# Performance work log

Measured on AMD Instinct MI355X. Metric: run time of the kernel, lower is better.

Reference implementation:

```python
import jax, jax.numpy as jnp
import numpy as np

N_NODES = 100000
N_EDGES = 600000
D = 128
N_GRAPHS = 128
EPS_GIN = 0.0      # GINConv eps (train_eps=False -> constant)
EPS_LN = 1e-5      # LayerNorm eps


def setup_inputs() -> dict:
    key = jax.random.key(0)
    ks = jax.random.split(key, 8)
    x = jax.random.normal(ks[0], (N_NODES, D), dtype=jnp.float32)
    edge_index = jax.random.randint(ks[1], (2, N_EDGES), 0, N_NODES, dtype=jnp.int64)
    batch = jnp.sort(jax.random.randint(ks[2], (N_NODES,), 0, N_GRAPHS, dtype=jnp.int64))
    # GIN update MLP: Linear(D,D) -> ReLU -> Linear(D,D)
    s = 1.0 / np.sqrt(D)
    W1 = jax.random.uniform(ks[3], (D, D), jnp.float32, -s, s)
    b1 = jax.random.uniform(ks[4], (D,), jnp.float32, -s, s)
    W2 = jax.random.uniform(ks[5], (D, D), jnp.float32, -s, s)
    b2 = jax.random.uniform(ks[6], (D,), jnp.float32, -s, s)
    # node LayerNorm affine params
    gamma = jnp.ones((D,), jnp.float32)
    beta = jnp.zeros((D,), jnp.float32)
    return {"x": x, "W1": W1, "b1": b1, "W2": W2, "b2": b2,
            "gamma": gamma, "beta": beta, "edge_index": edge_index, "batch": batch}


def reference(x, W1, b1, W2, b2, gamma, beta, edge_index, batch):
    src, dst = edge_index[0], edge_index[1]
    # AGGREGATION: m_i = sum_{j in N(i)} x_j  (scatter-sum of gathered source feats)
    m = jax.ops.segment_sum(x[src], dst, num_segments=N_NODES)  # [N, D]
    # UPDATE: MLP((1+eps)*x + m)
    h = (1.0 + EPS_GIN) * x + m
    h = jax.nn.relu(h @ W1 + b1) @ W2 + b2
    # node-mode LayerNorm: normalize each node over its feature dimension
    mu = jnp.mean(h, axis=-1, keepdims=True)
    var = jnp.mean((h - mu) ** 2, axis=-1, keepdims=True)
    return (h - mu) * jax.lax.rsqrt(var + EPS_LN) * gamma + beta
```

## Files before the change

kernel.cpp:

```cpp
#include <hip/hip_runtime.h>

#define NN 100000
#define NE 600000
#define DD 128
#define SCAN_BLOCKS 100
#define SCAN_CHUNK  1000

typedef __bf16 bf16x8 __attribute__((ext_vector_type(8)));
typedef float f32x4 __attribute__((ext_vector_type(4)));
typedef unsigned short ushort8 __attribute__((ext_vector_type(8)));

static __device__ __forceinline__ unsigned short f2bf(float f) {
    return __builtin_bit_cast(unsigned short, (__bf16)f);
}

__global__ void prep_w_kernel(const float* __restrict__ W1, const float* __restrict__ W2,
                              unsigned short* __restrict__ w1t, unsigned short* __restrict__ w2t) {
    int t = blockIdx.x * blockDim.x + threadIdx.x;
    int k = t >> 7, n = t & 127;
    w1t[n * DD + k] = f2bf(W1[k * DD + n]);
    w2t[n * DD + k] = f2bf(W2[k * DD + n]);
}

__global__ void hist_kernel(const int* __restrict__ ei, int* __restrict__ deg) {
    int e = blockIdx.x * blockDim.x + threadIdx.x;
    if (e < NE) atomicAdd(&deg[ei[NE + e]], 1);
}

__global__ void scanA_kernel(const int* __restrict__ deg, int* __restrict__ bsum) {
    __shared__ int red[256];
    int b = blockIdx.x, t = threadIdx.x;
    int base = b * SCAN_CHUNK;
    int s = 0;
    for (int i = t; i < SCAN_CHUNK; i += 256) s += deg[base + i];
    red[t] = s;
    __syncthreads();
    for (int off = 128; off > 0; off >>= 1) {
        if (t < off) red[t] += red[t + off];
        __syncthreads();
    }
    if (t == 0) bsum[b] = red[0];
}

__global__ void scanB_kernel(const int* __restrict__ bsum, int* __restrict__ boff) {
    __shared__ int s[128];
    int t = threadIdx.x;
    int v0 = (t < SCAN_BLOCKS) ? bsum[t] : 0;
    s[t] = v0;
    __syncthreads();
    for (int off = 1; off < 128; off <<= 1) {
        int u = (t >= off) ? s[t - off] : 0;
        __syncthreads();
        s[t] += u;
        __syncthreads();
    }
    if (t < SCAN_BLOCKS) boff[t] = s[t] - v0;
}

__global__ void scanC_kernel(const int* __restrict__ deg, const int* __restrict__ boff,
                             int* __restrict__ row_ptr, int* __restrict__ cursor) {
    __shared__ int s[1024];
    int b = blockIdx.x, t = threadIdx.x;
    int i = b * SCAN_CHUNK + t;
    int v = (t < SCAN_CHUNK) ? deg[i] : 0;
    s[t] = v;
    __syncthreads();
    for (int off = 1; off < 1024; off <<= 1) {
        int u = (t >= off) ? s[t - off] : 0;
        __syncthreads();
        s[t] += u;
        __syncthreads();
    }
    if (t < SCAN_CHUNK) {
        int excl = boff[b] + s[t] - v;
        row_ptr[i] = excl;
        cursor[i]  = excl;
        if (i == NN - 1) row_ptr[NN] = excl + v;
    }
}

__global__ void fill_kernel(const int* __restrict__ ei, int* __restrict__ cursor,
                            int* __restrict__ eidx) {
    int e = blockIdx.x * blockDim.x + threadIdx.x;
    if (e >= NE) return;
    int src = ei[e];
    int dst = ei[NE + e];
    int pos = atomicAdd(&cursor[dst], 1);
    eidx[pos] = src;
}

__global__ void gather_kernel(const float* __restrict__ x, const int* __restrict__ row_ptr,
                              const int* __restrict__ eidx, float* __restrict__ m) {
    int t = blockIdx.x * blockDim.x + threadIdx.x;
    int node = t >> 5;
    int j = (t & 31) * 4;
    if (node >= NN) return;
    int beg = row_ptr[node], end = row_ptr[node + 1];
    float4 acc = {0.f, 0.f, 0.f, 0.f};
    for (int e = beg; e < end; ++e) {
        int src = eidx[e];
        float4 v = *(const float4*)(x + (size_t)src * DD + j);
        acc.x += v.x; acc.y += v.y; acc.z += v.z; acc.w += v.w;
    }
    *(float4*)(m + (size_t)node * DD + j) = acc;
}

__launch_bounds__(256)
__global__ void fused_mlp_ln_kernel(const float* __restrict__ x, const float* __restrict__ m,
                                    const unsigned short* __restrict__ w1t,
                                    const unsigned short* __restrict__ w2t,
                                    const float* __restrict__ b1, const float* __restrict__ b2,
                                    const float* __restrict__ gamma, const float* __restrict__ beta,
                                    float* __restrict__ out) {
    __shared__ __align__(16) unsigned short h1[4][16][136];

    const int tid  = threadIdx.x;
    const int w    = tid >> 6;
    const int l    = tid & 63;
    const int lcol = l & 15;
    const int g    = l >> 4;
    const int m0   = blockIdx.x * 64 + w * 16;

    int arow = m0 + lcol;
    if (arow >= NN) arow = NN - 1;
    const float* xr = x + (size_t)arow * DD;
    const float* mr = m + (size_t)arow * DD;
    bf16x8 afrag[4];
    #pragma unroll
    for (int t = 0; t < 4; ++t) {
        int k0 = t * 32 + g * 8;
        float4 xa = *(const float4*)(xr + k0);
        float4 xb = *(const float4*)(xr + k0 + 4);
        float4 ma = *(const float4*)(mr + k0);
        float4 mb = *(const float4*)(mr + k0 + 4);
        bf16x8 a;
        a[0] = (__bf16)(xa.x + ma.x); a[1] = (__bf16)(xa.y + ma.y);
        a[2] = (__bf16)(xa.z + ma.z); a[3] = (__bf16)(xa.w + ma.w);
        a[4] = (__bf16)(xb.x + mb.x); a[5] = (__bf16)(xb.y + mb.y);
        a[6] = (__bf16)(xb.z + mb.z); a[7] = (__bf16)(xb.w + mb.w);
        afrag[t] = a;
    }

    f32x4 acc[8];
    #pragma unroll
    for (int nt = 0; nt < 8; ++nt) {
        float bv = b1[nt * 16 + lcol];
        acc[nt] = (f32x4){bv, bv, bv, bv};
    }
    #pragma unroll
    for (int t = 0; t < 4; ++t) {
        int k0 = t * 32 + g * 8;
        #pragma unroll
        for (int nt = 0; nt < 8; ++nt) {
            ushort8 bu = *(const ushort8*)(w1t + (size_t)(nt * 16 + lcol) * DD + k0);
            acc[nt] = __builtin_amdgcn_mfma_f32_16x16x32_bf16(
                afrag[t], __builtin_bit_cast(bf16x8, bu), acc[nt], 0, 0, 0);
        }
    }

    #pragma unroll
    for (int nt = 0; nt < 8; ++nt)
        #pragma unroll
        for (int r = 0; r < 4; ++r) {
            float v = fmaxf(acc[nt][r], 0.f);
            h1[w][g * 4 + r][nt * 16 + lcol] = f2bf(v);
        }
    __syncthreads();

    bf16x8 a2[4];
    #pragma unroll
    for (int t = 0; t < 4; ++t) {
        int k0 = t * 32 + g * 8;
        a2[t] = __builtin_bit_cast(bf16x8, *(const ushort8*)(&h1[w][lcol][k0]));
    }

    #pragma unroll
    for (int nt = 0; nt < 8; ++nt) {
        float bv = b2[nt * 16 + lcol];
        acc[nt] = (f32x4){bv, bv, bv, bv};
    }
    #pragma unroll
    for (int t = 0; t < 4; ++t) {
        #pragma unroll
        for (int nt = 0; nt < 8; ++nt) {
            ushort8 bu = *(const ushort8*)(w2t + (size_t)(nt * 16 + lcol) * DD + (t * 32 + g * 8));
            acc[nt] = __builtin_amdgcn_mfma_f32_16x16x32_bf16(
                a2[t], __builtin_bit_cast(bf16x8, bu), acc[nt], 0, 0, 0);
        }
    }

    float gmm[8], bta[8];
    #pragma unroll
    for (int nt = 0; nt < 8; ++nt) {
        gmm[nt] = gamma[nt * 16 + lcol];
        bta[nt] = beta[nt * 16 + lcol];
    }
    #pragma unroll
    for (int r = 0; r < 4; ++r) {
        int row = m0 + g * 4 + r;
        float s = 0.f, s2 = 0.f;
        #pragma unroll
        for (int nt = 0; nt < 8; ++nt) {
            float v = acc[nt][r];
            s += v; s2 += v * v;
        }
        #pragma unroll
        for (int msk = 1; msk < 16; msk <<= 1) {
            s  += __shfl_xor(s,  msk);
            s2 += __shfl_xor(s2, msk);
        }
        float mu  = s * (1.f / 128.f);
        float var = s2 * (1.f / 128.f) - mu * mu;
        float rs  = rsqrtf(var + 1e-5f);
        if (row < NN) {
            float* op = out + (size_t)row * DD;
            #pragma unroll
            for (int nt = 0; nt < 8; ++nt)
                op[nt * 16 + lcol] = (acc[nt][r] - mu) * rs * gmm[nt] + bta[nt];
        }
    }
}

extern "C" void kernel_launch(void* const* d_in, const int* in_sizes, int n_in,
                              void* d_out, int out_size, void* d_ws, size_t ws_size,
                              hipStream_t stream) {
    const float* x     = (const float*)d_in[0];
    const float* W1    = (const float*)d_in[1];
    const float* b1    = (const float*)d_in[2];
    const float* W2    = (const float*)d_in[3];
    const float* b2    = (const float*)d_in[4];
    const float* gamma = (const float*)d_in[5];
    const float* beta  = (const float*)d_in[6];
    const int*   ei    = (const int*)d_in[7];
    float* out = (float*)d_out;

    char* base = (char*)d_ws;
    float* m = (float*)base;                      base += (size_t)NN * DD * sizeof(float);
    unsigned short* w1t = (unsigned short*)base;  base += DD * DD * sizeof(unsigned short);
    unsigned short* w2t = (unsigned short*)base;  base += DD * DD * sizeof(unsigned short);
    int* deg     = (int*)base;                    base += NN * sizeof(int);
    int* cursor  = (int*)base;                    base += NN * sizeof(int);
    int* row_ptr = (int*)base;                    base += (NN + 1) * sizeof(int);
    int* eidx    = (int*)base;                    base += NE * sizeof(int);
    int* bsum    = (int*)base;                    base += 128 * sizeof(int);
    int* boff    = (int*)base;                    base += 128 * sizeof(int);

    hipMemsetAsync(deg, 0, NN * sizeof(int), stream);
    prep_w_kernel<<<(DD * DD) / 256, 256, 0, stream>>>(W1, W2, w1t, w2t);
    hist_kernel<<<(NE + 255) / 256, 256, 0, stream>>>(ei, deg);
    scanA_kernel<<<SCAN_BLOCKS, 256, 0, stream>>>(deg, bsum);
    scanB_kernel<<<1, 128, 0, stream>>>(bsum, boff);
    scanC_kernel<<<SCAN_BLOCKS, 1024, 0, stream>>>(deg, boff, row_ptr, cursor);
    fill_kernel<<<(NE + 255) / 256, 256, 0, stream>>>(ei, cursor, eidx);
    gather_kernel<<<(NN * 32 + 255) / 256, 256, 0, stream>>>(x, row_ptr, eidx, m);
    fused_mlp_ln_kernel<<<(NN + 63) / 64, 256, 0, stream>>>(
        x, m, w1t, w2t, b1, b2, gamma, beta, out);
}
```

Baseline: 292.7 us.

## Fuse neighbor gather-sum into MLP+LayerNorm kernel via shared-memory staging

Removes the separate gather kernel and the intermediate m buffer; each wave now aggregates neighbor features for its 16 rows directly into LDS as bf16, then feeds the MFMA MLP. This eliminates writing and re-reading a full N×D fp32 intermediate and one launch. It trades this for less memory-level parallelism per wave during the gather. The block barrier is also dropped, relying on per-wave buffer ownership.

```diff
diff --git a/kernel.cpp b/kernel.cpp
--- a/kernel.cpp
+++ b/kernel.cpp
@@ -89,30 +89,16 @@
     eidx[pos] = src;
 }
 
-__global__ void gather_kernel(const float* __restrict__ x, const int* __restrict__ row_ptr,
-                              const int* __restrict__ eidx, float* __restrict__ m) {
-    int t = blockIdx.x * blockDim.x + threadIdx.x;
-    int node = t >> 5;
-    int j = (t & 31) * 4;
-    if (node >= NN) return;
-    int beg = row_ptr[node], end = row_ptr[node + 1];
-    float4 acc = {0.f, 0.f, 0.f, 0.f};
-    for (int e = beg; e < end; ++e) {
-        int src = eidx[e];
-        float4 v = *(const float4*)(x + (size_t)src * DD + j);
-        acc.x += v.x; acc.y += v.y; acc.z += v.z; acc.w += v.w;
-    }
-    *(float4*)(m + (size_t)node * DD + j) = acc;
-}
-
 __launch_bounds__(256)
-__global__ void fused_mlp_ln_kernel(const float* __restrict__ x, const float* __restrict__ m,
-                                    const unsigned short* __restrict__ w1t,
-                                    const unsigned short* __restrict__ w2t,
-                                    const float* __restrict__ b1, const float* __restrict__ b2,
-                                    const float* __restrict__ gamma, const float* __restrict__ beta,
-                                    float* __restrict__ out) {
-    __shared__ __align__(16) unsigned short h1[4][16][136];
+__global__ void fused_gin_kernel(const float* __restrict__ x,
+                                 const int* __restrict__ row_ptr,
+                                 const int* __restrict__ eidx,
+                                 const unsigned short* __restrict__ w1t,
+                                 const unsigned short* __restrict__ w2t,
+                                 const float* __restrict__ b1, const float* __restrict__ b2,
+                                 const float* __restrict__ gamma, const float* __restrict__ beta,
+                                 float* __restrict__ out) {
+    __shared__ __align__(16) unsigned short buf[4][16][136];
 
     const int tid  = threadIdx.x;
     const int w    = tid >> 6;
@@ -121,24 +107,40 @@
     const int g    = l >> 4;
     const int m0   = blockIdx.x * 64 + w * 16;
 
-    int arow = m0 + lcol;
-    if (arow >= NN) arow = NN - 1;
-    const float* xr = x + (size_t)arow * DD;
-    const float* mr = m + (size_t)arow * DD;
+    {
+        const int c2 = l * 2;
+        #pragma unroll 2
+        for (int r = 0; r < 16; ++r) {
+            int row = m0 + r;
+            int beg = 0, end = 0;
+            if (row < NN) { beg = row_ptr[row]; end = row_ptr[row + 1]; }
+            int xrow = (row < NN) ? row : (NN - 1);
+            float2 acc = *(const float2*)(x + (size_t)xrow * DD + c2);
+            float2 acc2 = {0.f, 0.f};
+            int e = beg;
+            for (; e + 1 < end; e += 2) {
+                int s0 = eidx[e], s1 = eidx[e + 1];
+                float2 v0 = *(const float2*)(x + (size_t)s0 * DD + c2);
+                float2 v1 = *(const float2*)(x + (size_t)s1 * DD + c2);
+                acc.x  += v0.x; acc.y  += v0.y;
+                acc2.x += v1.x; acc2.y += v1.y;
+            }
+            if (e < end) {
+                int s0 = eidx[e];
+                float2 v0 = *(const float2*)(x + (size_t)s0 * DD + c2);
+                acc.x += v0.x; acc.y += v0.y;
+            }
+            acc.x += acc2.x; acc.y += acc2.y;
+            unsigned int packed = ((unsigned int)f2bf(acc.y) << 16) | (unsigned int)f2bf(acc.x);
+            *(unsigned int*)(&buf[w][r][c2]) = packed;
+        }
+    }
+
     bf16x8 afrag[4];
     #pragma unroll
     for (int t = 0; t < 4; ++t) {
         int k0 = t * 32 + g * 8;
-        float4 xa = *(const float4*)(xr + k0);
-        float4 xb = *(const float4*)(xr + k0 + 4);
-        float4 ma = *(const float4*)(mr + k0);
-        float4 mb = *(const float4*)(mr + k0 + 4);
-        bf16x8 a;
-        a[0] = (__bf16)(xa.x + ma.x); a[1] = (__bf16)(xa.y + ma.y);
-        a[2] = (__bf16)(xa.z + ma.z); a[3] = (__bf16)(xa.w + ma.w);
-        a[4] = (__bf16)(xb.x + mb.x); a[5] = (__bf16)(xb.y + mb.y);
-        a[6] = (__bf16)(xb.z + mb.z); a[7] = (__bf16)(xb.w + mb.w);
-        afrag[t] = a;
+        afrag[t] = __builtin_bit_cast(bf16x8, *(const ushort8*)(&buf[w][lcol][k0]));
     }
 
     f32x4 acc[8];
@@ -163,15 +165,14 @@
         #pragma unroll
         for (int r = 0; r < 4; ++r) {
             float v = fmaxf(acc[nt][r], 0.f);
-            h1[w][g * 4 + r][nt * 16 + lcol] = f2bf(v);
-        }
-    __syncthreads();
+            buf[w][g * 4 + r][nt * 16 + lcol] = f2bf(v);
+        }
 
     bf16x8 a2[4];
     #pragma unroll
     for (int t = 0; t < 4; ++t) {
         int k0 = t * 32 + g * 8;
-        a2[t] = __builtin_bit_cast(bf16x8, *(const ushort8*)(&h1[w][lcol][k0]));
+        a2[t] = __builtin_bit_cast(bf16x8, *(const ushort8*)(&buf[w][lcol][k0]));
     }
 
     #pragma unroll
@@ -235,7 +236,6 @@
     float* out = (float*)d_out;
 
     char* base = (char*)d_ws;
-    float* m = (float*)base;                      base += (size_t)NN * DD * sizeof(float);
     unsigned short* w1t = (unsigned short*)base;  base += DD * DD * sizeof(unsigned short);
     unsigned short* w2t = (unsigned short*)base;  base += DD * DD * sizeof(unsigned short);
     int* deg     = (int*)base;                    base += NN * sizeof(int);
@@ -252,7 +252,6 @@
     scanB_kernel<<<1, 128, 0, stream>>>(bsum, boff);
     scanC_kernel<<<SCAN_BLOCKS, 1024, 0, stream>>>(deg, boff, row_ptr, cursor);
     fill_kernel<<<(NE + 255) / 256, 256, 0, stream>>>(ei, cursor, eidx);
-    gather_kernel<<<(NN * 32 + 255) / 256, 256, 0, stream>>>(x, row_ptr, eidx, m);
-    fused_mlp_ln_kernel<<<(NN + 63) / 64, 256, 0, stream>>>(
-        x, m, w1t, w2t, b1, b2, gamma, beta, out);
-}
+    fused_gin_kernel<<<(NN + 63) / 64, 256, 0, stream>>>(
+        x, row_ptr, eidx, w1t, w2t, b1, b2, gamma, beta, out);
+}
```

New measurement: 353.0 us. 1.21x slower.
